# Optimization experiments

Hardware: AMD Instinct MI355X
Metric: run time of the kernel (lower is better)

The kernel has to match this reference:

```python
import jax, jax.numpy as jnp
import numpy as np
import math

LOG_EPS = -1000.0   # matches LOG_EPS in the torch source
NEG = -1e9          # stand-in for -inf (grad-safe)
T_MIN, T_MAX = 0.1, 1.0
GUMBEL_RATIO = 0.5  # gumbel_temperature_ratio forward arg (scalar float)


def setup_inputs() -> dict:
    key = jax.random.key(0)
    k1, k2, k3 = jax.random.split(key, 3)
    B, I, J, D = 4, 96, 384, 256
    return {
        "text_embeddings": jax.random.normal(k1, (B, I, D), jnp.float32),
        "mel_embeddings": jax.random.normal(k2, (B, J, D), jnp.float32),
        "gumbel_noise_u": jax.random.uniform(k3, (B, I, J), jnp.float32,
                                             minval=1e-6, maxval=1.0 - 1e-6),
        "text_mask": jnp.ones((B, I), dtype=bool),
        "mel_mask": jnp.ones((B, J), dtype=bool),
    }


def _soft_alignment(text_embeddings, mel_embeddings, gumbel_noise_u, text_mask, mel_mask):
    B, I, Dt = text_embeddings.shape
    _, J, Dm = mel_embeddings.shape

    # energy (B, I, J) = bmm / sqrt(D_text * D_mel)
    energy = jnp.einsum('bid,bjd->bij', text_embeddings, mel_embeddings) / math.sqrt(Dt * Dm)
    # gumbel noise + temperature
    temperature = T_MIN + (T_MAX - T_MIN) * GUMBEL_RATIO
    noise = -jnp.log(-jnp.log(gumbel_noise_u))
    energy = (energy + noise) / temperature

    len_t = text_mask.sum(1)  # (B,)
    len_m = mel_mask.sum(1)   # (B,)
    j_idx = jnp.arange(J)

    # invalid triangular mask (B, I, J, K): boundary j must not precede previous boundary k
    tri = j_idx[:, None] < j_idx[None, :]                       # (J, K)
    invalid = (tri[None, None]
               | ~text_mask[:, :, None, None]
               | ~mel_mask[:, None, :, None]
               | ~mel_mask[:, None, None, :])
    # force_assign_last: last text token's boundary forced to the last mel frame
    last_i = jnp.arange(I)[None, :] == (len_t - 1)[:, None]     # (B, I)
    not_last_j = j_idx[None, :] != (len_m - 1)[:, None]         # (B, J)
    invalid = invalid | (last_i[:, :, None, None] & not_last_j[:, None, :, None])

    # log conditional prob P(B_i = j | B_{i-1} = k), normalized over j (axis=2)
    e4 = jnp.where(invalid, LOG_EPS, energy[..., None])         # (B, I, J, K)
    log_cond_prob = e4 - jax.nn.logsumexp(e4, axis=2, keepdims=True)
    # reverse logcumsumexp over j: log P(B_i >= j | B_{i-1} = k)
    geq = jnp.flip(jax.lax.cumlogsumexp(jnp.flip(log_cond_prob, 2), axis=2), 2)
    geq = jnp.where(invalid, LOG_EPS, geq)

    # forward DP: B_ij (B, I+1, J+1), B_ij[:,0,0] = 0
    row0 = jnp.full((B, J + 1), NEG).at[:, 0].set(0.0)
    jj = jnp.arange(1, J + 1)

    def step(prev, inp):
        i, lcp = inp                                            # lcp: (B, J, K=J)
        # B_ij[b,i,j] = lse_k B_ij[b,i-1,k] + log_cond_prob[b,i-1,j-1,k]
        vals = jax.nn.logsumexp(prev[:, None, :-1] + lcp, axis=2)  # (B, J)
        window = (jj >= i) & (jj <= J - I + i + 1)              # only j in [i, J-I+i+1] written
        new = jnp.where(window[None, :], vals, NEG)
        new = jnp.concatenate([jnp.full((B, 1), NEG), new], axis=1)
        return new, new

    _, rows = jax.lax.scan(step, row0,
                           (jnp.arange(1, I + 1), jnp.swapaxes(log_cond_prob, 0, 1)))
    Bij = jnp.concatenate([row0[:, None, :], jnp.swapaxes(rows, 0, 1)], axis=1)  # (B, I+1, J+1)

    prob = Bij[:, :-1, :-1]                                     # (B, I, K)
    # log P(B_{i-1} < j <= B_i) = lse_k prob[b,i,k] + geq[b,i,j,k]
    log_boundary = jax.nn.logsumexp(prob[:, :, None, :] + geq, axis=3)  # (B, I, J)
    return log_boundary


def reference(text_embeddings, mel_embeddings, gumbel_noise_u, text_mask, mel_mask):
    soft = _soft_alignment(text_embeddings, mel_embeddings, gumbel_noise_u,
                           text_mask, mel_mask)
    # expanded text embeddings (B, J, D_text)
    expanded = jnp.einsum('bij,bid->bjd', jnp.exp(soft), text_embeddings)
    return soft, expanded
```

## Files before the change

kernel.cpp:

```cpp
#include <hip/hip_runtime.h>
#include <hip/hip_bf16.h>
#include <math.h>

#define B_ 4
#define I_ 96
#define J_ 384
#define D_ 256
#define NEG_     -1000000000.0f
#define NEGINF_  -3.0e38f
#define INV_TEMP_ (1.0f/0.55f)
#define LOG2E_   1.4426950408889634f
#define LN2_     0.6931471805599453f
#define LOGEPS2_ (-1000.0f*LOG2E_)

__device__ __forceinline__ float lse2(float a, float b) {
    float m = fmaxf(a, b);
    float d = fminf(a, b) - m;
    return m + __log2f(1.0f + __builtin_exp2f(d));
}

template<int CTRL, int RMASK = 0xF>
__device__ __forceinline__ float dpp_id(float x) {
    return __int_as_float(__builtin_amdgcn_update_dpp(
        __float_as_int(NEGINF_), __float_as_int(x), CTRL, RMASK, 0xF, false));
}
__device__ __forceinline__ float rdlane(float x, int l_const) {
    return __int_as_float(__builtin_amdgcn_readlane(__float_as_int(x), l_const));
}

__device__ __forceinline__ float wave_incl_prefix_lse(float x) {
    x = lse2(x, dpp_id<0x111>(x));
    x = lse2(x, dpp_id<0x112>(x));
    x = lse2(x, dpp_id<0x114>(x));
    x = lse2(x, dpp_id<0x118>(x));
    x = lse2(x, dpp_id<0x142, 0xa>(x));
    x = lse2(x, dpp_id<0x143, 0xc>(x));
    return x;
}
__device__ __forceinline__ float wave_incl_suffix_lse(float x, int lane) {
    x = lse2(x, dpp_id<0x101>(x));
    x = lse2(x, dpp_id<0x102>(x));
    x = lse2(x, dpp_id<0x104>(x));
    x = lse2(x, dpp_id<0x108>(x));
    float t1 = rdlane(x, 16), t2 = rdlane(x, 32), t3 = rdlane(x, 48);
    int row = lane >> 4;
    float u23 = lse2(t2, t3);
    float add = (row == 3) ? NEGINF_ : (row == 2) ? t3
              : (row == 1) ? u23 : lse2(t1, u23);
    return lse2(x, add);
}
__device__ __forceinline__ float combine_pre(const float* p, int w) {
    float l01 = lse2(p[0], p[1]);
    float l23 = lse2(p[2], p[3]);
    float P3 = lse2(l01, p[2]);
    float P4 = lse2(l01, l23);
    float P5 = lse2(P4, p[4]);
    return (w == 0) ? NEGINF_ : (w == 1) ? p[0] : (w == 2) ? l01
         : (w == 3) ? P3 : (w == 4) ? P4 : P5;
}
__device__ __forceinline__ float combine_suf(const float* s, int w) {
    float h45 = lse2(s[4], s[5]);
    float h23 = lse2(s[2], s[3]);
    float S3 = lse2(s[3], h45);
    float S2 = lse2(h23, h45);
    float S1 = lse2(s[1], S2);
    return (w == 5) ? NEGINF_ : (w == 4) ? s[5] : (w == 3) ? h45
         : (w == 2) ? S3 : (w == 1) ? S2 : S1;
}

__global__ __launch_bounds__(384) void k_energy(
    const float* __restrict__ text, const float* __restrict__ mel,
    const float* __restrict__ gum, float* __restrict__ Sarr,
    float* __restrict__ Earr)
{
    const int i = blockIdx.x, b = blockIdx.y;
    const int tid = threadIdx.x, lane = tid & 63, w = tid >> 6;
    __shared__ float4 tex4[D_/4];
    __shared__ float wtot[6];

    if (tid < D_/4)
        tex4[tid] = ((const float4*)(text + ((size_t)b*I_ + i)*D_))[tid];
    __syncthreads();

    const int j = tid;
    const float4* mrow = (const float4*)(mel + ((size_t)b*J_ + j)*D_);
    float acc = 0.f;
    #pragma unroll 8
    for (int d4 = 0; d4 < D_/4; ++d4) {
        float4 m4 = mrow[d4];
        float4 t4 = tex4[d4];
        acc += t4.x*m4.x + t4.y*m4.y + t4.z*m4.z + t4.w*m4.w;
    }
    float u = gum[((size_t)b*I_ + i)*J_ + j];
    float noise = -__logf(-__logf(u));
    float e2 = (acc * (1.0f/256.0f) + noise) * (INV_TEMP_ * LOG2E_);

    float sincl = wave_incl_suffix_lse(e2, lane);
    if (lane == 0) wtot[w] = sincl;
    __syncthreads();
    float sw = combine_suf(wtot, w);
    size_t off = ((size_t)b*I_ + i)*J_ + j;
    Sarr[off] = lse2(sincl, sw);
    Earr[off] = e2;
}

__global__ __launch_bounds__(64) void k_dp(
    const float* __restrict__ Sarr, const float* __restrict__ Earr,
    float* __restrict__ prob)
{
    const int b = blockIdx.x;
    const int lane = threadIdx.x;
    const int k0 = lane * 6;
    const float* Sb = Sarr + (size_t)b*I_*J_;
    const float* Eb = Earr + (size_t)b*I_*J_;
    float* Pb = prob + (size_t)b*I_*J_;

    float prev[6];
    #pragma unroll
    for (int t = 0; t < 6; ++t) {
        int k = k0 + t;
        float v0 = (k == 0) ? 0.0f : NEG_;
        prev[t] = v0;
        Pb[k] = v0;
    }

    float SA[6], EA[6], SBf[6], EBf[6];
    #pragma unroll
    for (int t = 0; t < 6; ++t) {
        int k = k0 + t;
        SA[t] = Sb[k];
        EA[t] = Eb[(k == 0) ? 0 : k - 1];
    }
    #pragma unroll
    for (int t = 0; t < 6; ++t) {
        int k = k0 + t;
        SBf[t] = Sb[(size_t)1*J_ + k];
        EBf[t] = Eb[(size_t)1*J_ + ((k == 0) ? 0 : k - 1)];
    }

    auto STEP = [&](int i, float* Sx, float* Ex, int loadrow) {
        float v[6], Ecur[6];
        #pragma unroll
        for (int t = 0; t < 6; ++t) { v[t] = prev[t] - Sx[t]; Ecur[t] = Ex[t]; }
        if (loadrow >= 0) {
            #pragma unroll
            for (int t = 0; t < 6; ++t) {
                int k = k0 + t;
                Sx[t] = Sb[(size_t)loadrow*J_ + k];
                Ex[t] = Eb[(size_t)loadrow*J_ + ((k == 0) ? 0 : k - 1)];
            }
        }
        float p[6];
        p[0] = v[0];
        #pragma unroll
        for (int t = 1; t < 6; ++t) p[t] = lse2(p[t-1], v[t]);
        float inc = wave_incl_prefix_lse(p[5]);
        float pexcl = dpp_id<0x138>(inc);
        float nv[6];
        nv[0] = pexcl + Ecur[0];
        #pragma unroll
        for (int t = 1; t < 6; ++t) nv[t] = lse2(pexcl, p[t-1]) + Ecur[t];
        float* Prow = Pb + (size_t)i*J_;
        #pragma unroll
        for (int t = 0; t < 6; ++t) {
            int k = k0 + t;
            bool win = (k >= i) && (k <= 289 + i);
            float val = win ? nv[t] : NEG_;
            prev[t] = val;
            Prow[k] = val;
        }
    };

    int i = 1;
    for (; i + 1 <= I_-1; i += 2) {
        STEP(i,     SA,  EA,  (i + 1 <= I_-2) ? i + 1 : -1);
        STEP(i + 1, SBf, EBf, (i + 2 <= I_-2) ? i + 2 : -1);
    }
    if (i == I_-1) STEP(i, SA, EA, -1);
}

__global__ __launch_bounds__(384) void k_soft(
    float* __restrict__ probsoft,
    const float* __restrict__ Sarr)
{
    const int i = blockIdx.x, b = blockIdx.y;
    const int tid = threadIdx.x, lane = tid & 63, w = tid >> 6;
    const int j = tid;
    __shared__ float tot[12];
    float* Row = probsoft + ((size_t)b*I_ + i)*J_;
    float p = Row[j];

    if (i == I_-1) {
        float sincl = wave_incl_suffix_lse(p, lane);
        if (lane == 0) tot[w] = sincl;
        __syncthreads();
        float m = tot[0];
        #pragma unroll
        for (int t = 1; t < 6; ++t) m = lse2(m, tot[t]);
        Row[j] = (j == J_-1) ? LN2_ * m : LN2_ * m - 1000.0f;
        return;
    }

    float S6 = Sarr[((size_t)b*I_ + i)*J_ + j];
    float v = p - S6;
    float qincl = wave_incl_prefix_lse(v);
    float tsuf  = wave_incl_suffix_lse(p, lane);
    if (lane == 63) tot[w] = qincl;
    if (lane == 0)  tot[6 + w] = tsuf;
    __syncthreads();
    float pt[6], st[6];
    #pragma unroll
    for (int t = 0; t < 6; ++t) { pt[t] = tot[t]; st[t] = tot[6+t]; }
    float Qful = lse2(combine_pre(pt, w), qincl);
    float Texw = dpp_id<0x130>(tsuf);
    float Texc = lse2(combine_suf(st, w), Texw);
    Row[j] = LN2_ * lse2(Qful + S6, Texc + LOGEPS2_);
}

__global__ __launch_bounds__(256) void k_expand(
    const float* __restrict__ soft, const float* __restrict__ text,
    float* __restrict__ out2)
{
    const int j = blockIdx.x, b = blockIdx.y;
    const int tid = threadIdx.x;
    __shared__ float wsh[I_];
    if (tid < I_) wsh[tid] = __expf(soft[((size_t)b*I_ + tid)*J_ + j]);
    __syncthreads();
    float acc = 0.f;
    const float* tcol = text + (size_t)b*I_*D_ + tid;
    #pragma unroll 8
    for (int i = 0; i < I_; ++i) acc += wsh[i] * tcol[(size_t)i*D_];
    out2[((size_t)b*J_ + j)*D_ + tid] = acc;
}

extern "C" void kernel_launch(void* const* d_in, const int* in_sizes, int n_in,
                              void* d_out, int out_size, void* d_ws, size_t ws_size,
                              hipStream_t stream) {
    const float* text = (const float*)d_in[0];
    const float* mel  = (const float*)d_in[1];
    const float* gum  = (const float*)d_in[2];

    float* out    = (float*)d_out;
    float* soft   = out;
    float* out2   = out + (size_t)B_*I_*J_;
    float* Sarr   = out2;
    float* Earr   = out2 + (size_t)B_*I_*J_;
    float* prob   = soft;

    k_energy<<<dim3(I_, B_), 384, 0, stream>>>(text, mel, gum, Sarr, Earr);
    k_dp    <<<dim3(B_),      64, 0, stream>>>(Sarr, Earr, prob);
    k_soft  <<<dim3(I_, B_), 384, 0, stream>>>(prob, Sarr);
    k_expand<<<dim3(J_, B_), 256, 0, stream>>>(soft, text, out2);
}
```

Baseline: 160.6 us.

## Fuse all stages into one cooperative kernel and shorten DP scan depth

Merges the four kernels (energy, sequential DP, soft boundary, expand) into one cooperative kernel with grid-wide syncs between phases, which removes the separate launches and the gaps between them. The expand phase is remapped onto the same 384 blocks, with each block handling 4 mel frames. Inside each DP step, the serial 6-element lse prefix chain becomes a log-depth scan, shortening the dependency chain on the latency-bound single-wave recurrence. In exchange it adds grid.sync overhead, requires every block to be co-resident, and leaves most blocks idle while the DP runs.

```diff
diff --git a/kernel.cpp b/kernel.cpp
--- a/kernel.cpp
+++ b/kernel.cpp
@@ -1,6 +1,9 @@
 #include <hip/hip_runtime.h>
+#include <hip/hip_cooperative_groups.h>
 #include <hip/hip_bf16.h>
 #include <math.h>
+
+namespace cg = cooperative_groups;
 
 #define B_ 4
 #define I_ 96
@@ -68,169 +71,169 @@
          : (w == 2) ? S3 : (w == 1) ? S2 : S1;
 }
 
-__global__ __launch_bounds__(384) void k_energy(
+__global__ __launch_bounds__(384) void k_fused(
     const float* __restrict__ text, const float* __restrict__ mel,
-    const float* __restrict__ gum, float* __restrict__ Sarr,
+    const float* __restrict__ gum, float* __restrict__ probsoft,
+    float* __restrict__ out2, float* __restrict__ Sarr,
     float* __restrict__ Earr)
 {
-    const int i = blockIdx.x, b = blockIdx.y;
+    cg::grid_group grid = cg::this_grid();
     const int tid = threadIdx.x, lane = tid & 63, w = tid >> 6;
+    const int blk = blockIdx.x;
+    const int b = blk / I_, i = blk % I_;
+
     __shared__ float4 tex4[D_/4];
-    __shared__ float wtot[6];
-
-    if (tid < D_/4)
-        tex4[tid] = ((const float4*)(text + ((size_t)b*I_ + i)*D_))[tid];
-    __syncthreads();
-
-    const int j = tid;
-    const float4* mrow = (const float4*)(mel + ((size_t)b*J_ + j)*D_);
-    float acc = 0.f;
-    #pragma unroll 8
-    for (int d4 = 0; d4 < D_/4; ++d4) {
-        float4 m4 = mrow[d4];
-        float4 t4 = tex4[d4];
-        acc += t4.x*m4.x + t4.y*m4.y + t4.z*m4.z + t4.w*m4.w;
-    }
-    float u = gum[((size_t)b*I_ + i)*J_ + j];
-    float noise = -__logf(-__logf(u));
-    float e2 = (acc * (1.0f/256.0f) + noise) * (INV_TEMP_ * LOG2E_);
-
-    float sincl = wave_incl_suffix_lse(e2, lane);
-    if (lane == 0) wtot[w] = sincl;
-    __syncthreads();
-    float sw = combine_suf(wtot, w);
-    size_t off = ((size_t)b*I_ + i)*J_ + j;
-    Sarr[off] = lse2(sincl, sw);
-    Earr[off] = e2;
-}
-
-__global__ __launch_bounds__(64) void k_dp(
-    const float* __restrict__ Sarr, const float* __restrict__ Earr,
-    float* __restrict__ prob)
-{
-    const int b = blockIdx.x;
-    const int lane = threadIdx.x;
-    const int k0 = lane * 6;
-    const float* Sb = Sarr + (size_t)b*I_*J_;
-    const float* Eb = Earr + (size_t)b*I_*J_;
-    float* Pb = prob + (size_t)b*I_*J_;
-
-    float prev[6];
-    #pragma unroll
-    for (int t = 0; t < 6; ++t) {
-        int k = k0 + t;
-        float v0 = (k == 0) ? 0.0f : NEG_;
-        prev[t] = v0;
-        Pb[k] = v0;
-    }
-
-    float SA[6], EA[6], SBf[6], EBf[6];
-    #pragma unroll
-    for (int t = 0; t < 6; ++t) {
-        int k = k0 + t;
-        SA[t] = Sb[k];
-        EA[t] = Eb[(k == 0) ? 0 : k - 1];
-    }
-    #pragma unroll
-    for (int t = 0; t < 6; ++t) {
-        int k = k0 + t;
-        SBf[t] = Sb[(size_t)1*J_ + k];
-        EBf[t] = Eb[(size_t)1*J_ + ((k == 0) ? 0 : k - 1)];
-    }
-
-    auto STEP = [&](int i, float* Sx, float* Ex, int loadrow) {
-        float v[6], Ecur[6];
-        #pragma unroll
-        for (int t = 0; t < 6; ++t) { v[t] = prev[t] - Sx[t]; Ecur[t] = Ex[t]; }
-        if (loadrow >= 0) {
-            #pragma unroll
-            for (int t = 0; t < 6; ++t) {
-                int k = k0 + t;
-                Sx[t] = Sb[(size_t)loadrow*J_ + k];
-                Ex[t] = Eb[(size_t)loadrow*J_ + ((k == 0) ? 0 : k - 1)];
-            }
-        }
-        float p[6];
-        p[0] = v[0];
-        #pragma unroll
-        for (int t = 1; t < 6; ++t) p[t] = lse2(p[t-1], v[t]);
-        float inc = wave_incl_prefix_lse(p[5]);
-        float pexcl = dpp_id<0x138>(inc);
-        float nv[6];
-        nv[0] = pexcl + Ecur[0];
-        #pragma unroll
-        for (int t = 1; t < 6; ++t) nv[t] = lse2(pexcl, p[t-1]) + Ecur[t];
-        float* Prow = Pb + (size_t)i*J_;
+    __shared__ float tot[12];
+    __shared__ float wsh[I_];
+
+    {
+        if (tid < D_/4)
+            tex4[tid] = ((const float4*)(text + ((size_t)b*I_ + i)*D_))[tid];
+        __syncthreads();
+        const int j = tid;
+        const float4* mrow = (const float4*)(mel + ((size_t)b*J_ + j)*D_);
+        float acc = 0.f;
+        #pragma unroll 8
+        for (int d4 = 0; d4 < D_/4; ++d4) {
+            float4 m4 = mrow[d4];
+            float4 t4 = tex4[d4];
+            acc += t4.x*m4.x + t4.y*m4.y + t4.z*m4.z + t4.w*m4.w;
+        }
+        float u = gum[((size_t)b*I_ + i)*J_ + j];
+        float noise = -__logf(-__logf(u));
+        float e2 = (acc * (1.0f/256.0f) + noise) * (INV_TEMP_ * LOG2E_);
+        float sincl = wave_incl_suffix_lse(e2, lane);
+        if (lane == 0) tot[w] = sincl;
+        __syncthreads();
+        float sw = combine_suf(tot, w);
+        size_t off = ((size_t)b*I_ + i)*J_ + j;
+        Sarr[off] = lse2(sincl, sw);
+        Earr[off] = e2;
+    }
+    grid.sync();
+
+    if (blk < B_ && tid < 64) {
+        const int k0 = lane * 6;
+        const float* Sb = Sarr + (size_t)blk*I_*J_;
+        const float* Eb = Earr + (size_t)blk*I_*J_;
+        float* Pb = probsoft + (size_t)blk*I_*J_;
+
+        float prev[6];
         #pragma unroll
         for (int t = 0; t < 6; ++t) {
             int k = k0 + t;
-            bool win = (k >= i) && (k <= 289 + i);
-            float val = win ? nv[t] : NEG_;
-            prev[t] = val;
-            Prow[k] = val;
-        }
-    };
-
-    int i = 1;
-    for (; i + 1 <= I_-1; i += 2) {
-        STEP(i,     SA,  EA,  (i + 1 <= I_-2) ? i + 1 : -1);
-        STEP(i + 1, SBf, EBf, (i + 2 <= I_-2) ? i + 2 : -1);
-    }
-    if (i == I_-1) STEP(i, SA, EA, -1);
-}
-
-__global__ __launch_bounds__(384) void k_soft(
-    float* __restrict__ probsoft,
-    const float* __restrict__ Sarr)
-{
-    const int i = blockIdx.x, b = blockIdx.y;
-    const int tid = threadIdx.x, lane = tid & 63, w = tid >> 6;
-    const int j = tid;
-    __shared__ float tot[12];
-    float* Row = probsoft + ((size_t)b*I_ + i)*J_;
-    float p = Row[j];
-
-    if (i == I_-1) {
-        float sincl = wave_incl_suffix_lse(p, lane);
-        if (lane == 0) tot[w] = sincl;
-        __syncthreads();
-        float m = tot[0];
+            float v0 = (k == 0) ? 0.0f : NEG_;
+            prev[t] = v0;
+            Pb[k] = v0;
+        }
+        float SA[6], EA[6], SBf[6], EBf[6];
         #pragma unroll
-        for (int t = 1; t < 6; ++t) m = lse2(m, tot[t]);
-        Row[j] = (j == J_-1) ? LN2_ * m : LN2_ * m - 1000.0f;
-        return;
-    }
-
-    float S6 = Sarr[((size_t)b*I_ + i)*J_ + j];
-    float v = p - S6;
-    float qincl = wave_incl_prefix_lse(v);
-    float tsuf  = wave_incl_suffix_lse(p, lane);
-    if (lane == 63) tot[w] = qincl;
-    if (lane == 0)  tot[6 + w] = tsuf;
-    __syncthreads();
-    float pt[6], st[6];
-    #pragma unroll
-    for (int t = 0; t < 6; ++t) { pt[t] = tot[t]; st[t] = tot[6+t]; }
-    float Qful = lse2(combine_pre(pt, w), qincl);
-    float Texw = dpp_id<0x130>(tsuf);
-    float Texc = lse2(combine_suf(st, w), Texw);
-    Row[j] = LN2_ * lse2(Qful + S6, Texc + LOGEPS2_);
-}
-
-__global__ __launch_bounds__(256) void k_expand(
-    const float* __restrict__ soft, const float* __restrict__ text,
-    float* __restrict__ out2)
-{
-    const int j = blockIdx.x, b = blockIdx.y;
-    const int tid = threadIdx.x;
-    __shared__ float wsh[I_];
-    if (tid < I_) wsh[tid] = __expf(soft[((size_t)b*I_ + tid)*J_ + j]);
-    __syncthreads();
-    float acc = 0.f;
-    const float* tcol = text + (size_t)b*I_*D_ + tid;
-    #pragma unroll 8
-    for (int i = 0; i < I_; ++i) acc += wsh[i] * tcol[(size_t)i*D_];
-    out2[((size_t)b*J_ + j)*D_ + tid] = acc;
+        for (int t = 0; t < 6; ++t) {
+            int k = k0 + t;
+            SA[t] = Sb[k];
+            EA[t] = Eb[(k == 0) ? 0 : k - 1];
+        }
+        #pragma unroll
+        for (int t = 0; t < 6; ++t) {
+            int k = k0 + t;
+            SBf[t] = Sb[(size_t)1*J_ + k];
+            EBf[t] = Eb[(size_t)1*J_ + ((k == 0) ? 0 : k - 1)];
+        }
+        auto STEP = [&](int ii, float* Sx, float* Ex, int loadrow) {
+            float v[6], Ecur[6];
+            #pragma unroll
+            for (int t = 0; t < 6; ++t) { v[t] = prev[t] - Sx[t]; Ecur[t] = Ex[t]; }
+            if (loadrow >= 0) {
+                #pragma unroll
+                for (int t = 0; t < 6; ++t) {
+                    int k = k0 + t;
+                    Sx[t] = Sb[(size_t)loadrow*J_ + k];
+                    Ex[t] = Eb[(size_t)loadrow*J_ + ((k == 0) ? 0 : k - 1)];
+                }
+            }
+            float p1[6], p2[6], p[6];
+            p1[0] = v[0];
+            #pragma unroll
+            for (int t = 1; t < 6; ++t) p1[t] = lse2(v[t-1], v[t]);
+            p2[0] = p1[0]; p2[1] = p1[1];
+            #pragma unroll
+            for (int t = 2; t < 6; ++t) p2[t] = lse2(p1[t-2], p1[t]);
+            p[0] = p2[0]; p[1] = p2[1]; p[2] = p2[2]; p[3] = p2[3];
+            p[4] = lse2(p2[0], p2[4]);
+            p[5] = lse2(p2[1], p2[5]);
+            float inc = wave_incl_prefix_lse(p[5]);
+            float pexcl = dpp_id<0x138>(inc);
+            float nv[6];
+            nv[0] = pexcl + Ecur[0];
+            #pragma unroll
+            for (int t = 1; t < 6; ++t) nv[t] = lse2(pexcl, p[t-1]) + Ecur[t];
+            float* Prow = Pb + (size_t)ii*J_;
+            #pragma unroll
+            for (int t = 0; t < 6; ++t) {
+                int k = k0 + t;
+                bool win = (k >= ii) && (k <= 289 + ii);
+                float val = win ? nv[t] : NEG_;
+                prev[t] = val;
+                Prow[k] = val;
+            }
+        };
+        int ii = 1;
+        for (; ii + 1 <= I_-1; ii += 2) {
+            STEP(ii,     SA,  EA,  (ii + 1 <= I_-2) ? ii + 1 : -1);
+            STEP(ii + 1, SBf, EBf, (ii + 2 <= I_-2) ? ii + 2 : -1);
+        }
+        if (ii == I_-1) STEP(ii, SA, EA, -1);
+    }
+    grid.sync();
+
+    {
+        const int j = tid;
+        float* Row = probsoft + ((size_t)b*I_ + i)*J_;
+        float p = Row[j];
+        if (i == I_-1) {
+            float sincl = wave_incl_suffix_lse(p, lane);
+            if (lane == 0) tot[w] = sincl;
+            __syncthreads();
+            float m = tot[0];
+            #pragma unroll
+            for (int t = 1; t < 6; ++t) m = lse2(m, tot[t]);
+            Row[j] = (j == J_-1) ? LN2_ * m : LN2_ * m - 1000.0f;
+        } else {
+            float S6 = Sarr[((size_t)b*I_ + i)*J_ + j];
+            float v = p - S6;
+            float qincl = wave_incl_prefix_lse(v);
+            float tsuf  = wave_incl_suffix_lse(p, lane);
+            if (lane == 63) tot[w] = qincl;
+            if (lane == 0)  tot[6 + w] = tsuf;
+            __syncthreads();
+            float pt[6], st[6];
+            #pragma unroll
+            for (int t = 0; t < 6; ++t) { pt[t] = tot[t]; st[t] = tot[6+t]; }
+            float Qful = lse2(combine_pre(pt, w), qincl);
+            float Texw = dpp_id<0x130>(tsuf);
+            float Texc = lse2(combine_suf(st, w), Texw);
+            Row[j] = LN2_ * lse2(Qful + S6, Texc + LOGEPS2_);
+        }
+    }
+    grid.sync();
+
+    {
+        const int eb = blk / 96, jbase = (blk % 96) * 4;
+        for (int jj = 0; jj < 4; ++jj) {
+            int j = jbase + jj;
+            __syncthreads();
+            if (tid < I_)
+                wsh[tid] = __expf(probsoft[((size_t)eb*I_ + tid)*J_ + j]);
+            __syncthreads();
+            if (tid < D_) {
+                float acc = 0.f;
+                const float* tcol = text + (size_t)eb*I_*D_ + tid;
+                #pragma unroll 8
+                for (int ii = 0; ii < I_; ++ii) acc += wsh[ii] * tcol[(size_t)ii*D_];
+                out2[((size_t)eb*J_ + j)*D_ + tid] = acc;
+            }
+        }
+    }
 }
 
 extern "C" void kernel_launch(void* const* d_in, const int* in_sizes, int n_in,
@@ -245,10 +248,9 @@
     float* out2   = out + (size_t)B_*I_*J_;
     float* Sarr   = out2;
     float* Earr   = out2 + (size_t)B_*I_*J_;
-    float* prob   = soft;
-
-    k_energy<<<dim3(I_, B_), 384, 0, stream>>>(text, mel, gum, Sarr, Earr);
-    k_dp    <<<dim3(B_),      64, 0, stream>>>(Sarr, Earr, prob);
-    k_soft  <<<dim3(I_, B_), 384, 0, stream>>>(prob, Sarr);
-    k_expand<<<dim3(J_, B_), 256, 0, stream>>>(soft, text, out2);
-}
+
+    void* args[] = { (void*)&text, (void*)&mel, (void*)&gum,
+                     (void*)&soft, (void*)&out2, (void*)&Sarr, (void*)&Earr };
+    hipLaunchCooperativeKernel((void*)k_fused, dim3(B_*I_), dim3(384),
+                               args, 0, stream);
+}
```

Result: slower. 297.9 us (+85.5%).
